# Kernel tuning notes

Measured on AMD Instinct MI355X. Metric: run time of the kernel, lower is better.

## Reference

```python
import jax, jax.numpy as jnp
import numpy as np

NUM_HEADS = 4
OUT_DIM = 64
IN_DIM = 128

def setup_inputs() -> dict:
    key = jax.random.key(0)
    k1, k2, k3, k4 = jax.random.split(key, 4)
    h = jax.random.normal(k1, (4, 256, IN_DIM), dtype=jnp.float32)
    adj = jax.random.randint(k2, (4, 256, 256), 0, 2).astype(jnp.int32)
    W = jax.random.normal(k3, (IN_DIM, NUM_HEADS * OUT_DIM), dtype=jnp.float32) * (1.0 / np.sqrt(IN_DIM))
    a = jax.random.normal(k4, (2 * OUT_DIM, 1), dtype=jnp.float32) * 0.1
    return {"h": h, "adj": adj, "W": W, "a": a}

def reference(h, adj, W, a):
    B, N, _ = h.shape
    H, D = NUM_HEADS, OUT_DIM
    Wh = (h @ W).reshape(B, N, H, D)                      # [B,N,H,D]
    # Exact replication of the torch repeat/view construction (row-major, same as torch.view)
    a1 = jnp.tile(Wh, (1, 1, 1, N)).reshape(B, N * H, N, D)
    a2 = jnp.tile(Wh, (1, N, 1, 1)).reshape(B, N * H, N, D)
    a_input = jnp.concatenate([a1, a2], axis=3)           # [B,N*H,N,2D]
    e = jax.nn.leaky_relu((a_input @ a)[..., 0], negative_slope=0.2)
    e = e.reshape(B, H, N, N)
    mask = adj[:, None, :, :] == 0                        # broadcast over heads
    attention = jax.nn.softmax(jnp.where(mask, -jnp.inf, e), axis=3)  # [B,H,N,N]
    h_prime = jnp.einsum('bhij,bjhd->bihd', attention, Wh)             # [B,N,H,D]
    return h_prime.reshape(B, N, H * D)
```

## Files before the change

kernel.cpp:

```cpp
#include <hip/hip_runtime.h>


typedef __attribute__((ext_vector_type(8))) short bf16x8;
typedef __attribute__((ext_vector_type(4))) float f32x4;

__device__ __forceinline__ short bf1(float x) {
  unsigned u = __builtin_bit_cast(unsigned, x);
  u = (u + 0x7FFFu + ((u >> 16) & 1u)) >> 16;
  return (short)u;
}
__device__ __forceinline__ bf16x8 pack8(float4 a, float4 b) {
  bf16x8 r;
  r[0]=bf1(a.x); r[1]=bf1(a.y); r[2]=bf1(a.z); r[3]=bf1(a.w);
  r[4]=bf1(b.x); r[5]=bf1(b.y); r[6]=bf1(b.z); r[7]=bf1(b.w);
  return r;
}

__global__ __launch_bounds__(512) void gat_fused(
    const float* __restrict__ h, const float* __restrict__ W,
    const float* __restrict__ a, const int* __restrict__ adj,
    float* __restrict__ out)
{
  const int tid  = threadIdx.x;
  const int lane = tid & 63;
  const int quad = lane >> 4;
  const int col  = lane & 15;
  const int wv   = tid >> 6;
  const int blk  = blockIdx.x;
  const int it = blk & 15, hp = (blk >> 4) & 3, b = blk >> 6;
  const int i0 = it * 16;

  __shared__ short WaTb[16][136];
  __shared__ short WbT[64][136];
  __shared__ float f2s[1024];
  __shared__ float f1v[16];
  __shared__ short attb[16][264];
  __shared__ float Ps[16][132];
  __shared__ float sinv[16];

  int4 adjv[2];
#pragma unroll
  for (int rq = 0; rq < 2; rq++) {
    const int i = i0 + wv * 2 + rq;
    adjv[rq] = *(const int4*)(adj + (b * 256 + i) * 256 + lane * 4);
  }

  {
    const int k = tid & 127, part = tid >> 7;
    const int sel = part >> 1, pair = part & 1;
    const float4* wrow = (const float4*)(W + k * 256 + pair * 128);
    const float4* ah = (const float4*)(a + sel * 64);
    float s0 = 0.f, s1 = 0.f;
#pragma unroll
    for (int d4 = 0; d4 < 16; d4++) {
      float4 x = wrow[d4]; float4 va = ah[d4];
      s0 += x.x*va.x + x.y*va.y + x.z*va.z + x.w*va.w;
    }
#pragma unroll
    for (int d4 = 0; d4 < 16; d4++) {
      float4 x = wrow[16 + d4]; float4 va = ah[d4];
      s1 += x.x*va.x + x.y*va.y + x.z*va.z + x.w*va.w;
    }
    const int row0 = sel * 4 + pair * 2;
    WaTb[row0 + 0][k] = bf1(s0);
    WaTb[row0 + 1][k] = bf1(s1);
    int* zp = (int*)&WaTb[8][0];
    for (int t = tid; t < 544; t += 512) zp[t] = 0;
  }
  {
#pragma unroll
    for (int q = 0; q < 4; q++) {
      const int idx = q * 512 + tid;
      const int k = idx >> 4, c4 = idx & 15;
      float4 w4 = *(const float4*)(W + k * 256 + hp * 64 + c4 * 4);
      WbT[c4*4 + 0][k] = bf1(w4.x);
      WbT[c4*4 + 1][k] = bf1(w4.y);
      WbT[c4*4 + 2][k] = bf1(w4.z);
      WbT[c4*4 + 3][k] = bf1(w4.w);
    }
  }
  __syncthreads();

  {
    bf16x8 bw[4];
#pragma unroll
    for (int kk = 0; kk < 4; kk++)
      bw[kk] = *(const bf16x8*)&WaTb[col][kk*32 + quad*8];
    const int mtstar = hp*4 + (it >> 2), qstar = it & 3;
#pragma unroll
    for (int q = 0; q < 2; q++) {
      const int mt = wv*2 + q, n0 = mt*16;
      const float* hrow = h + (b*256 + n0 + col)*128 + quad*8;
      f32x4 acc = {0.f, 0.f, 0.f, 0.f};
#pragma unroll
      for (int kk = 0; kk < 4; kk++) {
        float4 lo = *(const float4*)(hrow + kk*32);
        float4 hi = *(const float4*)(hrow + kk*32 + 4);
        acc = __builtin_amdgcn_mfma_f32_16x16x32_bf16(pack8(lo, hi), bw[kk], acc, 0, 0, 0);
      }
      if (col >= 4 && col < 8) {
#pragma unroll
        for (int r = 0; r < 4; r++) f2s[(n0 + quad*4 + r)*4 + (col - 4)] = acc[r];
      }
      if (mt == mtstar && col < 4 && quad == qstar) {
#pragma unroll
        for (int r = 0; r < 4; r++) f1v[r*4 + col] = acc[r];
      }
    }
  }
  __syncthreads();

#pragma unroll
  for (int rq = 0; rq < 2; rq++) {
    const int rr = wv*2 + rq;
    const int i  = i0 + rr;
    const float s1v = f1v[rr];
    float4 f2v = *(const float4*)(f2s + (i & 3)*256 + lane*4);
    const int4 av = adjv[rq];
    float e0 = s1v + f2v.x, e1 = s1v + f2v.y, e2 = s1v + f2v.z, e3 = s1v + f2v.w;
    e0 = e0 > 0.f ? e0 : 0.2f*e0;  e1 = e1 > 0.f ? e1 : 0.2f*e1;
    e2 = e2 > 0.f ? e2 : 0.2f*e2;  e3 = e3 > 0.f ? e3 : 0.2f*e3;
    e0 = av.x ? e0 : -1e30f;  e1 = av.y ? e1 : -1e30f;
    e2 = av.z ? e2 : -1e30f;  e3 = av.w ? e3 : -1e30f;
    float m = fmaxf(fmaxf(e0, e1), fmaxf(e2, e3));
#pragma unroll
    for (int off = 32; off > 0; off >>= 1) m = fmaxf(m, __shfl_xor(m, off, 64));
    float x0 = __expf(e0 - m), x1 = __expf(e1 - m);
    float x2 = __expf(e2 - m), x3 = __expf(e3 - m);
    float s = (x0 + x1) + (x2 + x3);
    float4 xa = {x0, x1, x2, x3};
    float4 xb = {0.f, 0.f, 0.f, 0.f};
    bf16x8 pk = pack8(xa, xb);
    *(int2*)&attb[rr][lane*4] = *(int2*)&pk;
#pragma unroll
    for (int off = 32; off > 0; off >>= 1) s += __shfl_xor(s, off, 64);
    if (lane == 0) sinv[rr] = 1.f / s;
  }
  __syncthreads();

  {
    bf16x8 af[8];
#pragma unroll
    for (int kk = 0; kk < 8; kk++)
      af[kk] = *(const bf16x8*)&attb[col][kk*32 + quad*8];
    const float* hcol = h + b*32768 + (wv*16 + col) + quad*8*128;
    f32x4 acc = {0.f, 0.f, 0.f, 0.f};
#pragma unroll
    for (int kk = 0; kk < 8; kk++) {
      const float* hq = hcol + kk*32*128;
      float4 lo = { hq[0],   hq[128], hq[256], hq[384] };
      float4 hi = { hq[512], hq[640], hq[768], hq[896] };
      acc = __builtin_amdgcn_mfma_f32_16x16x32_bf16(af[kk], pack8(lo, hi), acc, 0, 0, 0);
    }
#pragma unroll
    for (int r = 0; r < 4; r++) Ps[quad*4 + r][wv*16 + col] = acc[r];
  }
  __syncthreads();

  if (wv < 4) {
    f32x4 acc = {0.f, 0.f, 0.f, 0.f};
#pragma unroll
    for (int kk = 0; kk < 4; kk++) {
      float4 lo = *(const float4*)&Ps[col][kk*32 + quad*8];
      float4 hi = *(const float4*)&Ps[col][kk*32 + quad*8 + 4];
      bf16x8 bp = *(const bf16x8*)&WbT[wv*16 + col][kk*32 + quad*8];
      acc = __builtin_amdgcn_mfma_f32_16x16x32_bf16(pack8(lo, hi), bp, acc, 0, 0, 0);
    }
#pragma unroll
    for (int r = 0; r < 4; r++) {
      const int m = quad*4 + r;
      out[(b*256 + i0 + m)*256 + hp*64 + wv*16 + col] = acc[r] * sinv[m];
    }
  }
}

extern "C" void kernel_launch(void* const* d_in, const int* in_sizes, int n_in,
                              void* d_out, int out_size, void* d_ws, size_t ws_size,
                              hipStream_t stream) {
  const float* h   = (const float*)d_in[0];
  const int*   adj = (const int*)d_in[1];
  const float* W   = (const float*)d_in[2];
  const float* a   = (const float*)d_in[3];
  float* out = (float*)d_out;

  gat_fused<<<256, 512, 0, stream>>>(h, W, a, adj, out);
}
```

Measured before the change: 76.66 us.

## Precompute bf16 and transposed bf16 copies of h in a prep kernel

Adds a pre-pass kernel that converts h to bf16 in both row-major and transposed layouts in workspace. The fused kernel then loads packed bf16x8 vectors directly instead of doing strided fp32 gathers and per-element conversion, which cuts global traffic and the scattered column loads of h. The intermediate P tile is also stored in LDS as bf16 to halve shared memory use and skip a repack. The trade-offs are an extra kernel launch, a workspace round trip, and a scattered transpose write in the prep kernel.

New measurement: 79.63 us. +3.9%, slower.

```diff
diff --git a/kernel.cpp b/kernel.cpp
--- a/kernel.cpp
+++ b/kernel.cpp
@@ -16,10 +16,27 @@
   return r;
 }
 
+__global__ __launch_bounds__(256) void h_bf16_prep(
+    const float* __restrict__ h, short* __restrict__ hb, short* __restrict__ hTb)
+{
+  const int idx = blockIdx.x * 256 + threadIdx.x;
+  const int e0  = idx * 8;
+  const int b   = e0 >> 15;
+  const int r   = e0 & 32767;
+  const int n   = r >> 7, d0 = r & 127;
+  float4 lo = *(const float4*)(h + e0);
+  float4 hi = *(const float4*)(h + e0 + 4);
+  bf16x8 v = pack8(lo, hi);
+  *(bf16x8*)(hb + e0) = v;
+  short* tp = hTb + b * 32768 + d0 * 256 + n;
+#pragma unroll
+  for (int j = 0; j < 8; j++) tp[j * 256] = v[j];
+}
+
 __global__ __launch_bounds__(512) void gat_fused(
-    const float* __restrict__ h, const float* __restrict__ W,
-    const float* __restrict__ a, const int* __restrict__ adj,
-    float* __restrict__ out)
+    const short* __restrict__ hb, const short* __restrict__ hTb,
+    const float* __restrict__ W, const float* __restrict__ a,
+    const int* __restrict__ adj, float* __restrict__ out)
 {
   const int tid  = threadIdx.x;
   const int lane = tid & 63;
@@ -35,7 +52,7 @@
   __shared__ float f2s[1024];
   __shared__ float f1v[16];
   __shared__ short attb[16][264];
-  __shared__ float Ps[16][132];
+  __shared__ short Ps16[16][136];
   __shared__ float sinv[16];
 
   int4 adjv[2];
@@ -90,13 +107,12 @@
 #pragma unroll
     for (int q = 0; q < 2; q++) {
       const int mt = wv*2 + q, n0 = mt*16;
-      const float* hrow = h + (b*256 + n0 + col)*128 + quad*8;
+      const short* hrow = hb + (b*256 + n0 + col)*128 + quad*8;
       f32x4 acc = {0.f, 0.f, 0.f, 0.f};
 #pragma unroll
       for (int kk = 0; kk < 4; kk++) {
-        float4 lo = *(const float4*)(hrow + kk*32);
-        float4 hi = *(const float4*)(hrow + kk*32 + 4);
-        acc = __builtin_amdgcn_mfma_f32_16x16x32_bf16(pack8(lo, hi), bw[kk], acc, 0, 0, 0);
+        bf16x8 av = *(const bf16x8*)(hrow + kk*32);
+        acc = __builtin_amdgcn_mfma_f32_16x16x32_bf16(av, bw[kk], acc, 0, 0, 0);
       }
       if (col >= 4 && col < 8) {
 #pragma unroll
@@ -128,10 +144,10 @@
     float x0 = __expf(e0 - m), x1 = __expf(e1 - m);
     float x2 = __expf(e2 - m), x3 = __expf(e3 - m);
     float s = (x0 + x1) + (x2 + x3);
-    float4 xa = {x0, x1, x2, x3};
-    float4 xb = {0.f, 0.f, 0.f, 0.f};
-    bf16x8 pk = pack8(xa, xb);
-    *(int2*)&attb[rr][lane*4] = *(int2*)&pk;
+    unsigned w0 = (unsigned)(unsigned short)bf1(x0) | ((unsigned)(unsigned short)bf1(x1) << 16);
+    unsigned w1 = (unsigned)(unsigned short)bf1(x2) | ((unsigned)(unsigned short)bf1(x3) << 16);
+    int2 pk2; pk2.x = (int)w0; pk2.y = (int)w1;
+    *(int2*)&attb[rr][lane*4] = pk2;
 #pragma unroll
     for (int off = 32; off > 0; off >>= 1) s += __shfl_xor(s, off, 64);
     if (lane == 0) sinv[rr] = 1.f / s;
@@ -143,17 +159,16 @@
 #pragma unroll
     for (int kk = 0; kk < 8; kk++)
       af[kk] = *(const bf16x8*)&attb[col][kk*32 + quad*8];
-    const float* hcol = h + b*32768 + (wv*16 + col) + quad*8*128;
+    const short* hTrow = hTb + b*32768 + (wv*16 + col)*256 + quad*8;
     f32x4 acc = {0.f, 0.f, 0.f, 0.f};
 #pragma unroll
     for (int kk = 0; kk < 8; kk++) {
-      const float* hq = hcol + kk*32*128;
-      float4 lo = { hq[0],   hq[128], hq[256], hq[384] };
-      float4 hi = { hq[512], hq[640], hq[768], hq[896] };
-      acc = __builtin_amdgcn_mfma_f32_16x16x32_bf16(af[kk], pack8(lo, hi), acc, 0, 0, 0);
-    }
-#pragma unroll
-    for (int r = 0; r < 4; r++) Ps[quad*4 + r][wv*16 + col] = acc[r];
+      bf16x8 bv = *(const bf16x8*)(hTrow + kk*32);
+      acc = __builtin_amdgcn_mfma_f32_16x16x32_bf16(af[kk], bv, acc, 0, 0, 0);
+    }
+#pragma unroll
+    for (int r = 0; r < 4; r++)
+      Ps16[quad*4 + r][wv*16 + col] = bf1(acc[r]);
   }
   __syncthreads();
 
@@ -161,10 +176,9 @@
     f32x4 acc = {0.f, 0.f, 0.f, 0.f};
 #pragma unroll
     for (int kk = 0; kk < 4; kk++) {
-      float4 lo = *(const float4*)&Ps[col][kk*32 + quad*8];
-      float4 hi = *(const float4*)&Ps[col][kk*32 + quad*8 + 4];
+      bf16x8 ap = *(const bf16x8*)&Ps16[col][kk*32 + quad*8];
       bf16x8 bp = *(const bf16x8*)&WbT[wv*16 + col][kk*32 + quad*8];
-      acc = __builtin_amdgcn_mfma_f32_16x16x32_bf16(pack8(lo, hi), bp, acc, 0, 0, 0);
+      acc = __builtin_amdgcn_mfma_f32_16x16x32_bf16(ap, bp, acc, 0, 0, 0);
     }
 #pragma unroll
     for (int r = 0; r < 4; r++) {
@@ -183,5 +197,9 @@
   const float* a   = (const float*)d_in[3];
   float* out = (float*)d_out;
 
-  gat_fused<<<256, 512, 0, stream>>>(h, W, a, adj, out);
-}
+  short* hb  = (short*)d_ws;
+  short* hTb = hb + 4*256*128;
+
+  h_bf16_prep<<<64, 256, 0, stream>>>(h, hb, hTb);
+  gat_fused<<<256, 512, 0, stream>>>(hb, hTb, W, a, adj, out);
+}
```

## Split fused GAT kernel into Wh precompute and attention kernels via workspace

Applied to the files above, without the earlier changes.

Replaces the single fused kernel, which recomputed W projections and f1/f2 in every block and ran attention over raw h followed by a second W GEMM, with two kernels. A prep kernel computes Wh once per batch, stores it transposed as bf16 in workspace, and derives f1/f2 from that result with shuffle reductions. The attention kernel then handles 32 rows per block and multiplies attention directly by Wh. This removes redundant per-block projection work and the strided gathers of h, at the cost of an extra launch and a global round-trip for Wh, f1 and f2.

New measurement: 71.96 us. -6.1%, faster.

```diff
diff --git a/kernel.cpp b/kernel.cpp
--- a/kernel.cpp
+++ b/kernel.cpp
@@ -16,107 +16,111 @@
   return r;
 }
 
-__global__ __launch_bounds__(512) void gat_fused(
+__global__ __launch_bounds__(512) void gat_prep(
     const float* __restrict__ h, const float* __restrict__ W,
-    const float* __restrict__ a, const int* __restrict__ adj,
-    float* __restrict__ out)
+    const float* __restrict__ a,
+    short* __restrict__ WhT, float* __restrict__ f1g, float* __restrict__ f2g)
 {
   const int tid  = threadIdx.x;
   const int lane = tid & 63;
-  const int quad = lane >> 4;
-  const int col  = lane & 15;
+  const int quad = lane >> 4, col = lane & 15;
   const int wv   = tid >> 6;
   const int blk  = blockIdx.x;
-  const int it = blk & 15, hp = (blk >> 4) & 3, b = blk >> 6;
-  const int i0 = it * 16;
+  const int nt = blk & 3, mt = (blk >> 2) & 3, b = blk >> 4;
 
-  __shared__ short WaTb[16][136];
   __shared__ short WbT[64][136];
-  __shared__ float f2s[1024];
-  __shared__ float f1v[16];
-  __shared__ short attb[16][264];
-  __shared__ float Ps[16][132];
-  __shared__ float sinv[16];
+  __shared__ float f1p[64][4];
+  __shared__ float f2p[64][4];
 
-  int4 adjv[2];
 #pragma unroll
-  for (int rq = 0; rq < 2; rq++) {
-    const int i = i0 + wv * 2 + rq;
-    adjv[rq] = *(const int4*)(adj + (b * 256 + i) * 256 + lane * 4);
-  }
-
-  {
-    const int k = tid & 127, part = tid >> 7;
-    const int sel = part >> 1, pair = part & 1;
-    const float4* wrow = (const float4*)(W + k * 256 + pair * 128);
-    const float4* ah = (const float4*)(a + sel * 64);
-    float s0 = 0.f, s1 = 0.f;
-#pragma unroll
-    for (int d4 = 0; d4 < 16; d4++) {
-      float4 x = wrow[d4]; float4 va = ah[d4];
-      s0 += x.x*va.x + x.y*va.y + x.z*va.z + x.w*va.w;
-    }
-#pragma unroll
-    for (int d4 = 0; d4 < 16; d4++) {
-      float4 x = wrow[16 + d4]; float4 va = ah[d4];
-      s1 += x.x*va.x + x.y*va.y + x.z*va.z + x.w*va.w;
-    }
-    const int row0 = sel * 4 + pair * 2;
-    WaTb[row0 + 0][k] = bf1(s0);
-    WaTb[row0 + 1][k] = bf1(s1);
-    int* zp = (int*)&WaTb[8][0];
-    for (int t = tid; t < 544; t += 512) zp[t] = 0;
-  }
-  {
-#pragma unroll
-    for (int q = 0; q < 4; q++) {
-      const int idx = q * 512 + tid;
-      const int k = idx >> 4, c4 = idx & 15;
-      float4 w4 = *(const float4*)(W + k * 256 + hp * 64 + c4 * 4);
-      WbT[c4*4 + 0][k] = bf1(w4.x);
-      WbT[c4*4 + 1][k] = bf1(w4.y);
-      WbT[c4*4 + 2][k] = bf1(w4.z);
-      WbT[c4*4 + 3][k] = bf1(w4.w);
-    }
+  for (int q = 0; q < 4; q++) {
+    const int idx = q * 512 + tid;
+    const int k = idx >> 4, c4 = idx & 15;
+    float4 w4 = *(const float4*)(W + k * 256 + nt * 64 + c4 * 4);
+    WbT[c4*4 + 0][k] = bf1(w4.x);
+    WbT[c4*4 + 1][k] = bf1(w4.y);
+    WbT[c4*4 + 2][k] = bf1(w4.z);
+    WbT[c4*4 + 3][k] = bf1(w4.w);
   }
   __syncthreads();
 
-  {
-    bf16x8 bw[4];
+  const int tc = wv & 3;
+  const float a1v = a[tc*16 + col];
+  const float a2v = a[64 + tc*16 + col];
+
 #pragma unroll
-    for (int kk = 0; kk < 4; kk++)
-      bw[kk] = *(const bf16x8*)&WaTb[col][kk*32 + quad*8];
-    const int mtstar = hp*4 + (it >> 2), qstar = it & 3;
+  for (int q = 0; q < 2; q++) {
+    const int tr = (wv >> 2) * 2 + q;
+    const float* hrow = h + (b*256 + mt*64 + tr*16 + col) * 128 + quad*8;
+    f32x4 acc = {0.f, 0.f, 0.f, 0.f};
 #pragma unroll
-    for (int q = 0; q < 2; q++) {
-      const int mt = wv*2 + q, n0 = mt*16;
-      const float* hrow = h + (b*256 + n0 + col)*128 + quad*8;
-      f32x4 acc = {0.f, 0.f, 0.f, 0.f};
+    for (int kk = 0; kk < 4; kk++) {
+      float4 lo = *(const float4*)(hrow + kk*32);
+      float4 hi = *(const float4*)(hrow + kk*32 + 4);
+      bf16x8 bw = *(const bf16x8*)&WbT[tc*16 + col][kk*32 + quad*8];
+      acc = __builtin_amdgcn_mfma_f32_16x16x32_bf16(pack8(lo, hi), bw, acc, 0, 0, 0);
+    }
+    {
+      const int dcol = nt*64 + tc*16 + col;
+      const int n0   = mt*64 + tr*16 + quad*4;
+      int2 pk;
+      pk.x = (int)((unsigned)(unsigned short)bf1(acc[0]) |
+                   ((unsigned)(unsigned short)bf1(acc[1]) << 16));
+      pk.y = (int)((unsigned)(unsigned short)bf1(acc[2]) |
+                   ((unsigned)(unsigned short)bf1(acc[3]) << 16));
+      *(int2*)(WhT + b*65536 + dcol*256 + n0) = pk;
+    }
 #pragma unroll
-      for (int kk = 0; kk < 4; kk++) {
-        float4 lo = *(const float4*)(hrow + kk*32);
-        float4 hi = *(const float4*)(hrow + kk*32 + 4);
-        acc = __builtin_amdgcn_mfma_f32_16x16x32_bf16(pack8(lo, hi), bw[kk], acc, 0, 0, 0);
+    for (int r = 0; r < 4; r++) {
+      float v1 = acc[r] * a1v;
+      float v2 = acc[r] * a2v;
+#pragma unroll
+      for (int off = 1; off < 16; off <<= 1) {
+        v1 += __shfl_xor(v1, off, 64);
+        v2 += __shfl_xor(v2, off, 64);
       }
-      if (col >= 4 && col < 8) {
-#pragma unroll
-        for (int r = 0; r < 4; r++) f2s[(n0 + quad*4 + r)*4 + (col - 4)] = acc[r];
-      }
-      if (mt == mtstar && col < 4 && quad == qstar) {
-#pragma unroll
-        for (int r = 0; r < 4; r++) f1v[r*4 + col] = acc[r];
+      if (col == 0) {
+        const int row = tr*16 + quad*4 + r;
+        f1p[row][tc] = v1;
+        f2p[row][tc] = v2;
       }
     }
   }
   __syncthreads();
 
+  if (tid < 64) {
+    const float s = f1p[tid][0] + f1p[tid][1] + f1p[tid][2] + f1p[tid][3];
+    f1g[b*1024 + (mt*64 + tid)*4 + nt] = s;
+  } else if (tid < 128) {
+    const int n = tid - 64;
+    const float s = f2p[n][0] + f2p[n][1] + f2p[n][2] + f2p[n][3];
+    f2g[b*1024 + (mt*64 + n)*4 + nt] = s;
+  }
+}
+
+__global__ __launch_bounds__(512) void gat_attn(
+    const short* __restrict__ WhT, const float* __restrict__ f1g,
+    const float* __restrict__ f2g, const int* __restrict__ adj,
+    float* __restrict__ out)
+{
+  const int tid  = threadIdx.x;
+  const int lane = tid & 63;
+  const int quad = lane >> 4, col = lane & 15;
+  const int wv   = tid >> 6;
+  const int blk  = blockIdx.x;
+  const int it2 = blk & 7, hp = (blk >> 3) & 3, b = blk >> 5;
+  const int i0 = it2 * 32;
+
+  __shared__ short attb[32][264];
+  __shared__ float sinv[32];
+
 #pragma unroll
-  for (int rq = 0; rq < 2; rq++) {
-    const int rr = wv*2 + rq;
+  for (int rq = 0; rq < 4; rq++) {
+    const int rr = wv*4 + rq;
     const int i  = i0 + rr;
-    const float s1v = f1v[rr];
-    float4 f2v = *(const float4*)(f2s + (i & 3)*256 + lane*4);
-    const int4 av = adjv[rq];
+    const float s1v = f1g[b*1024 + hp*256 + i];
+    float4 f2v = *(const float4*)(f2g + b*1024 + (i & 3)*256 + lane*4);
+    int4 av = *(const int4*)(adj + (b*256 + i)*256 + lane*4);
     float e0 = s1v + f2v.x, e1 = s1v + f2v.y, e2 = s1v + f2v.z, e3 = s1v + f2v.w;
     e0 = e0 > 0.f ? e0 : 0.2f*e0;  e1 = e1 > 0.f ? e1 : 0.2f*e1;
     e2 = e2 > 0.f ? e2 : 0.2f*e2;  e3 = e3 > 0.f ? e3 : 0.2f*e3;
@@ -128,49 +132,34 @@
     float x0 = __expf(e0 - m), x1 = __expf(e1 - m);
     float x2 = __expf(e2 - m), x3 = __expf(e3 - m);
     float s = (x0 + x1) + (x2 + x3);
-    float4 xa = {x0, x1, x2, x3};
-    float4 xb = {0.f, 0.f, 0.f, 0.f};
-    bf16x8 pk = pack8(xa, xb);
-    *(int2*)&attb[rr][lane*4] = *(int2*)&pk;
+    int2 pk2;
+    pk2.x = (int)((unsigned)(unsigned short)bf1(x0) |
+                  ((unsigned)(unsigned short)bf1(x1) << 16));
+    pk2.y = (int)((unsigned)(unsigned short)bf1(x2) |
+                  ((unsigned)(unsigned short)bf1(x3) << 16));
+    *(int2*)&attb[rr][lane*4] = pk2;
 #pragma unroll
     for (int off = 32; off > 0; off >>= 1) s += __shfl_xor(s, off, 64);
     if (lane == 0) sinv[rr] = 1.f / s;
   }
   __syncthreads();
 
-  {
-    bf16x8 af[8];
+  const int rt = wv >> 2, ct = wv & 3;
+  bf16x8 af[8];
 #pragma unroll
-    for (int kk = 0; kk < 8; kk++)
-      af[kk] = *(const bf16x8*)&attb[col][kk*32 + quad*8];
-    const float* hcol = h + b*32768 + (wv*16 + col) + quad*8*128;
-    f32x4 acc = {0.f, 0.f, 0.f, 0.f};
+  for (int kk = 0; kk < 8; kk++)
+    af[kk] = *(const bf16x8*)&attb[rt*16 + col][kk*32 + quad*8];
+  const short* bp = WhT + b*65536 + (hp*64 + ct*16 + col)*256 + quad*8;
+  f32x4 acc = {0.f, 0.f, 0.f, 0.f};
 #pragma unroll
-    for (int kk = 0; kk < 8; kk++) {
-      const float* hq = hcol + kk*32*128;
-      float4 lo = { hq[0],   hq[128], hq[256], hq[384] };
-      float4 hi = { hq[512], hq[640], hq[768], hq[896] };
-      acc = __builtin_amdgcn_mfma_f32_16x16x32_bf16(af[kk], pack8(lo, hi), acc, 0, 0, 0);
-    }
+  for (int kk = 0; kk < 8; kk++) {
+    bf16x8 bv = *(const bf16x8*)(bp + kk*32);
+    acc = __builtin_amdgcn_mfma_f32_16x16x32_bf16(af[kk], bv, acc, 0, 0, 0);
+  }
 #pragma unroll
-    for (int r = 0; r < 4; r++) Ps[quad*4 + r][wv*16 + col] = acc[r];
-  }
-  __syncthreads();
-
-  if (wv < 4) {
-    f32x4 acc = {0.f, 0.f, 0.f, 0.f};
-#pragma unroll
-    for (int kk = 0; kk < 4; kk++) {
-      float4 lo = *(const float4*)&Ps[col][kk*32 + quad*8];
-      float4 hi = *(const float4*)&Ps[col][kk*32 + quad*8 + 4];
-      bf16x8 bp = *(const bf16x8*)&WbT[wv*16 + col][kk*32 + quad*8];
-      acc = __builtin_amdgcn_mfma_f32_16x16x32_bf16(pack8(lo, hi), bp, acc, 0, 0, 0);
-    }
-#pragma unroll
-    for (int r = 0; r < 4; r++) {
-      const int m = quad*4 + r;
-      out[(b*256 + i0 + m)*256 + hp*64 + wv*16 + col] = acc[r] * sinv[m];
-    }
+  for (int r = 0; r < 4; r++) {
+    const int m = rt*16 + quad*4 + r;
+    out[(b*256 + i0 + m)*256 + hp*64 + ct*16 + col] = acc[r] * sinv[m];
   }
 }
 
@@ -183,5 +172,10 @@
   const float* a   = (const float*)d_in[3];
   float* out = (float*)d_out;
 
-  gat_fused<<<256, 512, 0, stream>>>(h, W, a, adj, out);
+  short* WhT = (short*)d_ws;
+  float* f1g = (float*)((char*)d_ws + 4*256*256*2);
+  float* f2g = f1g + 4*1024;
+
+  gat_prep<<<64, 512, 0, stream>>>(h, W, a, WhT, f1g, f2g);
+  gat_attn<<<128, 512, 0, stream>>>(WhT, f1g, f2g, adj, out);
 }
```

## Compute Wh tile in LDS and fold row-sum into MFMA, halve block size

Applied to the files above, without the earlier changes.

The kernel now computes the per-head Wh = h·W slice for all 256 nodes inside each block and stores it transposed and XOR-swizzled in LDS as bf16. Attention is then applied directly to Wh, replacing the old attention·h followed by ·W chain, its strided column gathers of h, and the fp32 Ps staging buffer. Softmax drops the max-subtraction and cross-lane reductions: row sums come from an extra MFMA against a ones vector, and normalisation happens at the output. Blocks shrink to 256 threads with four rows per wave. In exchange, each block recomputes the full Wh projection redundantly, and dropping the max subtraction risks exp overflow when logits are large.

Result: faster. 69.44 us (-9.4%).

```diff
diff --git a/kernel.cpp b/kernel.cpp
--- a/kernel.cpp
+++ b/kernel.cpp
@@ -16,15 +16,14 @@
   return r;
 }
 
-__global__ __launch_bounds__(512) void gat_fused(
+__global__ __launch_bounds__(256) void gat_fused(
     const float* __restrict__ h, const float* __restrict__ W,
     const float* __restrict__ a, const int* __restrict__ adj,
     float* __restrict__ out)
 {
   const int tid  = threadIdx.x;
   const int lane = tid & 63;
-  const int quad = lane >> 4;
-  const int col  = lane & 15;
+  const int quad = lane >> 4, col = lane & 15;
   const int wv   = tid >> 6;
   const int blk  = blockIdx.x;
   const int it = blk & 15, hp = (blk >> 4) & 3, b = blk >> 6;
@@ -32,45 +31,46 @@
 
   __shared__ short WaTb[16][136];
   __shared__ short WbT[64][136];
+  __shared__ short WhTl[64][256];
   __shared__ float f2s[1024];
   __shared__ float f1v[16];
   __shared__ short attb[16][264];
-  __shared__ float Ps[16][132];
-  __shared__ float sinv[16];
-
-  int4 adjv[2];
-#pragma unroll
-  for (int rq = 0; rq < 2; rq++) {
-    const int i = i0 + wv * 2 + rq;
-    adjv[rq] = *(const int4*)(adj + (b * 256 + i) * 256 + lane * 4);
-  }
-
-  {
-    const int k = tid & 127, part = tid >> 7;
-    const int sel = part >> 1, pair = part & 1;
-    const float4* wrow = (const float4*)(W + k * 256 + pair * 128);
-    const float4* ah = (const float4*)(a + sel * 64);
-    float s0 = 0.f, s1 = 0.f;
+
+  int4 adjv[4];
+#pragma unroll
+  for (int rq = 0; rq < 4; rq++)
+    adjv[rq] = *(const int4*)(adj + (b*256 + i0 + wv*4 + rq)*256 + lane*4);
+
+  {
+    const int k = tid & 127, su = tid >> 7;
+    const float4* wrow = (const float4*)(W + k * 256 + su * 128);
+    const float4* a4 = (const float4*)a;
+    float s10 = 0.f, s11 = 0.f, s20 = 0.f, s21 = 0.f;
 #pragma unroll
     for (int d4 = 0; d4 < 16; d4++) {
-      float4 x = wrow[d4]; float4 va = ah[d4];
-      s0 += x.x*va.x + x.y*va.y + x.z*va.z + x.w*va.w;
+      float4 x = wrow[d4];
+      float4 v1 = a4[d4], v2 = a4[16 + d4];
+      s10 += x.x*v1.x + x.y*v1.y + x.z*v1.z + x.w*v1.w;
+      s20 += x.x*v2.x + x.y*v2.y + x.z*v2.z + x.w*v2.w;
     }
 #pragma unroll
     for (int d4 = 0; d4 < 16; d4++) {
-      float4 x = wrow[16 + d4]; float4 va = ah[d4];
-      s1 += x.x*va.x + x.y*va.y + x.z*va.z + x.w*va.w;
-    }
-    const int row0 = sel * 4 + pair * 2;
-    WaTb[row0 + 0][k] = bf1(s0);
-    WaTb[row0 + 1][k] = bf1(s1);
+      float4 x = wrow[16 + d4];
+      float4 v1 = a4[d4], v2 = a4[16 + d4];
+      s11 += x.x*v1.x + x.y*v1.y + x.z*v1.z + x.w*v1.w;
+      s21 += x.x*v2.x + x.y*v2.y + x.z*v2.z + x.w*v2.w;
+    }
+    WaTb[su*2 + 0][k] = bf1(s10);
+    WaTb[su*2 + 1][k] = bf1(s11);
+    WaTb[4 + su*2 + 0][k] = bf1(s20);
+    WaTb[4 + su*2 + 1][k] = bf1(s21);
     int* zp = (int*)&WaTb[8][0];
-    for (int t = tid; t < 544; t += 512) zp[t] = 0;
-  }
-  {
-#pragma unroll
-    for (int q = 0; q < 4; q++) {
-      const int idx = q * 512 + tid;
+    for (int t = tid; t < 544; t += 256) zp[t] = 0;
+  }
+  {
+#pragma unroll
+    for (int q = 0; q < 8; q++) {
+      const int idx = q * 256 + tid;
       const int k = idx >> 4, c4 = idx & 15;
       float4 w4 = *(const float4*)(W + k * 256 + hp * 64 + c4 * 4);
       WbT[c4*4 + 0][k] = bf1(w4.x);
@@ -82,59 +82,79 @@
   __syncthreads();
 
   {
-    bf16x8 bw[4];
+    bf16x8 waf[4];
 #pragma unroll
     for (int kk = 0; kk < 4; kk++)
-      bw[kk] = *(const bf16x8*)&WaTb[col][kk*32 + quad*8];
+      waf[kk] = *(const bf16x8*)&WaTb[col][kk*32 + quad*8];
+    bf16x8 wbf[4][4];
+#pragma unroll
+    for (int dt = 0; dt < 4; dt++)
+#pragma unroll
+      for (int kk = 0; kk < 4; kk++)
+        wbf[dt][kk] = *(const bf16x8*)&WbT[dt*16 + col][kk*32 + quad*8];
+
     const int mtstar = hp*4 + (it >> 2), qstar = it & 3;
 #pragma unroll
-    for (int q = 0; q < 2; q++) {
-      const int mt = wv*2 + q, n0 = mt*16;
+    for (int q = 0; q < 4; q++) {
+      const int mt = wv*4 + q, n0 = mt*16;
       const float* hrow = h + (b*256 + n0 + col)*128 + quad*8;
-      f32x4 acc = {0.f, 0.f, 0.f, 0.f};
+      bf16x8 afr[4];
 #pragma unroll
       for (int kk = 0; kk < 4; kk++) {
         float4 lo = *(const float4*)(hrow + kk*32);
         float4 hi = *(const float4*)(hrow + kk*32 + 4);
-        acc = __builtin_amdgcn_mfma_f32_16x16x32_bf16(pack8(lo, hi), bw[kk], acc, 0, 0, 0);
-      }
+        afr[kk] = pack8(lo, hi);
+      }
+      f32x4 accF = {0.f, 0.f, 0.f, 0.f};
+#pragma unroll
+      for (int kk = 0; kk < 4; kk++)
+        accF = __builtin_amdgcn_mfma_f32_16x16x32_bf16(afr[kk], waf[kk], accF, 0, 0, 0);
       if (col >= 4 && col < 8) {
 #pragma unroll
-        for (int r = 0; r < 4; r++) f2s[(n0 + quad*4 + r)*4 + (col - 4)] = acc[r];
+        for (int r = 0; r < 4; r++) f2s[(n0 + quad*4 + r)*4 + (col - 4)] = accF[r];
       }
       if (mt == mtstar && col < 4 && quad == qstar) {
 #pragma unroll
-        for (int r = 0; r < 4; r++) f1v[r*4 + col] = acc[r];
+        for (int r = 0; r < 4; r++) f1v[r*4 + col] = accF[r];
+      }
+#pragma unroll
+      for (int dt = 0; dt < 4; dt++) {
+        f32x4 aw = {0.f, 0.f, 0.f, 0.f};
+#pragma unroll
+        for (int kk = 0; kk < 4; kk++)
+          aw = __builtin_amdgcn_mfma_f32_16x16x32_bf16(afr[kk], wbf[dt][kk], aw, 0, 0, 0);
+        unsigned byteoff = (unsigned)((dt*16 + col) << 9) + (unsigned)((n0 + quad*4) << 1);
+        byteoff ^= (unsigned)(col & 7) << 4;
+        int2 pk;
+        pk.x = (int)((unsigned)(unsigned short)bf1(aw[0]) |
+                     ((unsigned)(unsigned short)bf1(aw[1]) << 16));
+        pk.y = (int)((unsigned)(unsigned short)bf1(aw[2]) |
+                     ((unsigned)(unsigned short)bf1(aw[3]) << 16));
+        *(int2*)((char*)&WhTl[0][0] + byteoff) = pk;
       }
     }
   }
   __syncthreads();
 
 #pragma unroll
-  for (int rq = 0; rq < 2; rq++) {
-    const int rr = wv*2 + rq;
-    const int i  = i0 + rr;
+  for (int rq = 0; rq < 4; rq++) {
+    const int rr = wv*4 + rq;
     const float s1v = f1v[rr];
-    float4 f2v = *(const float4*)(f2s + (i & 3)*256 + lane*4);
-    const int4 av = adjv[rq];
-    float e0 = s1v + f2v.x, e1 = s1v + f2v.y, e2 = s1v + f2v.z, e3 = s1v + f2v.w;
+    float4 f2v = *(const float4*)&f2s[rq*256 + lane*4];
+    float e0 = s1v + f2v.x, e1 = s1v + f2v.y;
+    float e2 = s1v + f2v.z, e3 = s1v + f2v.w;
     e0 = e0 > 0.f ? e0 : 0.2f*e0;  e1 = e1 > 0.f ? e1 : 0.2f*e1;
     e2 = e2 > 0.f ? e2 : 0.2f*e2;  e3 = e3 > 0.f ? e3 : 0.2f*e3;
-    e0 = av.x ? e0 : -1e30f;  e1 = av.y ? e1 : -1e30f;
-    e2 = av.z ? e2 : -1e30f;  e3 = av.w ? e3 : -1e30f;
-    float m = fmaxf(fmaxf(e0, e1), fmaxf(e2, e3));
-#pragma unroll
-    for (int off = 32; off > 0; off >>= 1) m = fmaxf(m, __shfl_xor(m, off, 64));
-    float x0 = __expf(e0 - m), x1 = __expf(e1 - m);
-    float x2 = __expf(e2 - m), x3 = __expf(e3 - m);
-    float s = (x0 + x1) + (x2 + x3);
-    float4 xa = {x0, x1, x2, x3};
-    float4 xb = {0.f, 0.f, 0.f, 0.f};
-    bf16x8 pk = pack8(xa, xb);
-    *(int2*)&attb[rr][lane*4] = *(int2*)&pk;
-#pragma unroll
-    for (int off = 32; off > 0; off >>= 1) s += __shfl_xor(s, off, 64);
-    if (lane == 0) sinv[rr] = 1.f / s;
+    e0 = adjv[rq].x ? e0 : -1e30f;  e1 = adjv[rq].y ? e1 : -1e30f;
+    e2 = adjv[rq].z ? e2 : -1e30f;  e3 = adjv[rq].w ? e3 : -1e30f;
+    float x0 = __expf(e0), x1 = __expf(e1);
+    float x2 = __expf(e2), x3 = __expf(e3);
+    int2 pk2;
+    pk2.x = (int)((unsigned)(unsigned short)bf1(x0) |
+                  ((unsigned)(unsigned short)bf1(x1) << 16));
+    pk2.y = (int)((unsigned)(unsigned short)bf1(x2) |
+                  ((unsigned)(unsigned short)bf1(x3) << 16));
+    *(int2*)&attb[rr][lane*4] = pk2;
   }
   __syncthreads();
 
@@ -143,33 +163,34 @@
 #pragma unroll
     for (int kk = 0; kk < 8; kk++)
       af[kk] = *(const bf16x8*)&attb[col][kk*32 + quad*8];
-    const float* hcol = h + b*32768 + (wv*16 + col) + quad*8*128;
-    f32x4 acc = {0.f, 0.f, 0.f, 0.f};
+
+    bf16x8 bv[8];
 #pragma unroll
     for (int kk = 0; kk < 8; kk++) {
-      const float* hq = hcol + kk*32*128;
-      float4 lo = { hq[0],   hq[128], hq[256], hq[384] };
-      float4 hi = { hq[512], hq[640], hq[768], hq[896] };
-      acc = __builtin_amdgcn_mfma_f32_16x16x32_bf16(af[kk], pack8(lo, hi), acc, 0, 0, 0);
-    }
-#pragma unroll
-    for (int r = 0; r < 4; r++) Ps[quad*4 + r][wv*16 + col] = acc[r];
-  }
-  __syncthreads();
-
-  if (wv < 4) {
-    f32x4 acc = {0.f, 0.f, 0.f, 0.f};
+      unsigned byteoff = (unsigned)((wv*16 + col) << 9) +
+                         (unsigned)((quad*8 + kk*32) << 1);
+      byteoff ^= (unsigned)(col & 7) << 4;
+      bv[kk] = *(const bf16x8*)((const char*)&WhTl[0][0] + byteoff);
+    }
+
+    bf16x8 ones;
+#pragma unroll
+    for (int j = 0; j < 8; j++) ones[j] = (short)0x3F80;
+
+    f32x4 acc0 = {0.f,0.f,0.f,0.f}, acc1 = {0.f,0.f,0.f,0.f};
+    f32x4 sum0 = {0.f,0.f,0.f,0.f}, sum1 = {0.f,0.f,0.f,0.f};
 #pragma unroll
     for (int kk = 0; kk < 4; kk++) {
-      float4 lo = *(const float4*)&Ps[col][kk*32 + quad*8];
-      float4 hi = *(const float4*)&Ps[col][kk*32 + quad*8 + 4];
-      bf16x8 bp = *(const bf16x8*)&WbT[wv*16 + col][kk*32 + quad*8];
-      acc = __builtin_amdgcn_mfma_f32_16x16x32_bf16(pack8(lo, hi), bp, acc, 0, 0, 0);
+      acc0 = __builtin_amdgcn_mfma_f32_16x16x32_bf16(af[kk],   bv[kk],   acc0, 0, 0, 0);
+      acc1 = __builtin_amdgcn_mfma_f32_16x16x32_bf16(af[kk+4], bv[kk+4], acc1, 0, 0, 0);
+      sum0 = __builtin_amdgcn_mfma_f32_16x16x32_bf16(af[kk],   ones,     sum0, 0, 0, 0);
+      sum1 = __builtin_amdgcn_mfma_f32_16x16x32_bf16(af[kk+4], ones,     sum1, 0, 0, 0);
     }
 #pragma unroll
     for (int r = 0; r < 4; r++) {
       const int m = quad*4 + r;
-      out[(b*256 + i0 + m)*256 + hp*64 + wv*16 + col] = acc[r] * sinv[m];
+      out[(b*256 + i0 + m)*256 + hp*64 + wv*16 + col] =
+          (acc0[r] + acc1[r]) / (sum0[r] + sum1[r]);
     }
   }
 }
@@ -183,5 +204,5 @@
   const float* a   = (const float*)d_in[3];
   float* out = (float*)d_out;
 
-  gat_fused<<<256, 512, 0, stream>>>(h, W, a, adj, out);
-}
+  gat_fused<<<256, 256, 0, stream>>>(h, W, a, adj, out);
+}
```
